# Kernel optimization log

Hardware: AMD Instinct MI355X
Metric: run time of the kernel (lower is better)

## Reference

```python
import jax, jax.numpy as jnp
import numpy as np


def setup_inputs() -> dict:
    key = jax.random.key(0)
    ks = jax.random.split(key, 7)
    B, D, N, R = 256, 5120, 16, 160  # batch, d_inner, d_state, dt_rank
    x = jax.random.normal(ks[0], (B, D), jnp.float32)
    h0 = jax.random.normal(ks[1], (B, D, N), jnp.float32)
    W_x_dt = jax.random.normal(ks[2], (D, R), jnp.float32) * (1.0 / np.sqrt(D))
    W_dt = jax.random.normal(ks[3], (R, D), jnp.float32) * (1.0 / np.sqrt(R))
    b_dt = jax.random.normal(ks[4], (D,), jnp.float32)
    W_BC = jax.random.normal(ks[5], (D, 2 * N), jnp.float32) * (1.0 / np.sqrt(D))
    A_log = jax.random.normal(ks[6], (D, N), jnp.float32)
    return {"x": x, "h0": h0, "W_x_dt": W_x_dt, "W_dt": W_dt,
            "b_dt": b_dt, "W_BC": W_BC, "A_log": A_log}


def reference(x, h0, W_x_dt, W_dt, b_dt, W_BC, A_log):
    # Single-token Mamba selective SSM step (batch dims squeezed: x [B,D], h0 [B,D,N]).
    N = A_log.shape[1]
    # delta_t = softplus(dt_proj(delta_t_proj(x)))  -> [B, D]
    dt = jax.nn.softplus((x @ W_x_dt) @ W_dt + b_dt)
    # BC projection, split into B and C parts -> [B, N] each
    BC = x @ W_BC
    Bm, Cm = BC[:, :N], BC[:, N:]
    A = -jnp.exp(A_log)                              # [D, N]
    delta_A = jnp.exp(A[None, :, :] * dt[:, :, None])   # [B, D, N]
    delta_Bx = (dt * x)[:, :, None] * Bm[:, None, :]     # [B, D, N]
    h = delta_A * h0 + delta_Bx                          # new hidden state
    # y = h @ C (per-batch bmm over state dim) + x residual
    y = jnp.einsum('bdn,bn->bd', h, Cm) + x              # [B, D]
    return y
```

## Files before the change

### kernel.cpp

```cpp
#include <hip/hip_runtime.h>
#include <math.h>

#define BB 256
#define DD 5120
#define NN 16
#define RR 160
#define CT 192
#define NSPLIT 32
#define TMP_ELEMS (BB * CT)
#define NEGA_ELEMS (DD * NN)

__global__ __launch_bounds__(256) void k1_gemm(const float* __restrict__ x,
                                               const float* __restrict__ Wxdt,
                                               const float* __restrict__ Wbc,
                                               float* __restrict__ part) {
    __shared__ float xs[32][68];
    __shared__ float ws[32][64];
    const int tid = threadIdx.x;
    const int tx = tid & 15, ty = tid >> 4;
    const int c0 = blockIdx.x * 64;
    const int b0 = blockIdx.y * 64;
    const int k0 = blockIdx.z * 160;
    float acc[4][4] = {};

    for (int kc = 0; kc < 160; kc += 32) {
        {
            const int i  = tid >> 3;
            const int j4 = (tid & 7) * 4;
            #pragma unroll
            for (int rep = 0; rep < 2; ++rep) {
                const int row = i + rep * 32;
                const float4 v = *(const float4*)&x[(size_t)(b0 + row) * DD + k0 + kc + j4];
                xs[j4 + 0][row] = v.x;
                xs[j4 + 1][row] = v.y;
                xs[j4 + 2][row] = v.z;
                xs[j4 + 3][row] = v.w;
            }
        }
        {
            const int c4 = (tid & 15) * 4;
            const int r0 = tid >> 4;
            #pragma unroll
            for (int rep = 0; rep < 2; ++rep) {
                const int r  = r0 + rep * 16;
                const int kg = k0 + kc + r;
                const int cg = c0 + c4;
                float4 v;
                if (cg < RR) v = *(const float4*)&Wxdt[(size_t)kg * RR + cg];
                else         v = *(const float4*)&Wbc[(size_t)kg * 32 + (cg - RR)];
                *(float4*)&ws[r][c4] = v;
            }
        }
        __syncthreads();
        #pragma unroll
        for (int k = 0; k < 32; ++k) {
            const float4 a4 = *(const float4*)&xs[k][ty * 4];
            const float4 w4 = *(const float4*)&ws[k][tx * 4];
            const float av[4] = {a4.x, a4.y, a4.z, a4.w};
            const float wv[4] = {w4.x, w4.y, w4.z, w4.w};
            #pragma unroll
            for (int u = 0; u < 4; ++u)
                #pragma unroll
                for (int v = 0; v < 4; ++v)
                    acc[u][v] = fmaf(av[u], wv[v], acc[u][v]);
        }
        __syncthreads();
    }

    float* p = part + (size_t)blockIdx.z * TMP_ELEMS;
    #pragma unroll
    for (int u = 0; u < 4; ++u) {
        const int b = b0 + ty * 4 + u;
        *(float4*)&p[b * CT + c0 + tx * 4] =
            make_float4(acc[u][0], acc[u][1], acc[u][2], acc[u][3]);
    }
}

__global__ __launch_bounds__(256) void k_red(const float* __restrict__ part,
                                             const float* __restrict__ Alog,
                                             float* __restrict__ tmp,
                                             float* __restrict__ negA) {
    const int idx = blockIdx.x * 256 + threadIdx.x;
    if (idx < TMP_ELEMS) {
        float s = 0.f;
        #pragma unroll
        for (int z = 0; z < NSPLIT; ++z) s += part[(size_t)z * TMP_ELEMS + idx];
        tmp[idx] = s;
    } else {
        const int j = idx - TMP_ELEMS;
        negA[j] = -__expf(Alog[j]);
    }
}

__global__ __launch_bounds__(256) void k_fused(const float* __restrict__ x,
                                               const float* __restrict__ h0,
                                               const float* __restrict__ Wdt,
                                               const float* __restrict__ bdt,
                                               const float* __restrict__ tmp,
                                               const float* __restrict__ negA,
                                               float* __restrict__ out) {
    const int tid = threadIdx.x;
    const int b0 = blockIdx.x * 4;
    const int d0 = blockIdx.y * 256;
    const int d  = d0 + tid;
    const float* wcol = Wdt + d;

    float acc[4] = {0.f, 0.f, 0.f, 0.f};
    #pragma unroll 4
    for (int k4 = 0; k4 < RR; k4 += 4) {
        const float w0 = wcol[(size_t)(k4 + 0) * DD];
        const float w1 = wcol[(size_t)(k4 + 1) * DD];
        const float w2 = wcol[(size_t)(k4 + 2) * DD];
        const float w3 = wcol[(size_t)(k4 + 3) * DD];
        #pragma unroll
        for (int bi = 0; bi < 4; ++bi) {
            const float4 t4 = *(const float4*)&tmp[(size_t)(b0 + bi) * CT + k4];
            acc[bi] = fmaf(t4.x, w0, acc[bi]);
            acc[bi] = fmaf(t4.y, w1, acc[bi]);
            acc[bi] = fmaf(t4.z, w2, acc[bi]);
            acc[bi] = fmaf(t4.w, w3, acc[bi]);
        }
    }

    const float bdv = bdt[d];
    float dtv[4];
    #pragma unroll
    for (int bi = 0; bi < 4; ++bi) {
        const float z = acc[bi] + bdv;
        dtv[bi] = fmaxf(z, 0.f) + log1pf(__expf(-fabsf(z)));
    }

    float av[16];
    {
        const float* ap = &negA[(size_t)d * NN];
        #pragma unroll
        for (int n4 = 0; n4 < NN; n4 += 4) {
            const float4 a4 = *(const float4*)&ap[n4];
            av[n4 + 0] = a4.x; av[n4 + 1] = a4.y;
            av[n4 + 2] = a4.z; av[n4 + 3] = a4.w;
        }
    }

    #pragma unroll
    for (int bi = 0; bi < 4; ++bi) {
        const size_t cell = (size_t)(b0 + bi) * DD + d;
        const float dt  = dtv[bi];
        const float xe  = x[cell];
        const float dtx = dt * xe;
        const float* hp  = &h0[cell * NN];
        const float* bmp = &tmp[(size_t)(b0 + bi) * CT + RR];
        float acc4[4] = {xe, 0.f, 0.f, 0.f};
        #pragma unroll
        for (int n4 = 0; n4 < NN; n4 += 4) {
            const float4 h4 = *(const float4*)&hp[n4];
            const float hv[4] = {h4.x, h4.y, h4.z, h4.w};
            #pragma unroll
            for (int q = 0; q < 4; ++q) {
                const int n = n4 + q;
                const float dA = __expf(av[n] * dt);
                const float h  = fmaf(dA, hv[q], dtx * bmp[n]);
                acc4[q] = fmaf(h, bmp[16 + n], acc4[q]);
            }
        }
        out[cell] = (acc4[0] + acc4[1]) + (acc4[2] + acc4[3]);
    }
}

extern "C" void kernel_launch(void* const* d_in, const int* in_sizes, int n_in,
                              void* d_out, int out_size, void* d_ws, size_t ws_size,
                              hipStream_t stream) {
    const float* x    = (const float*)d_in[0];
    const float* h0   = (const float*)d_in[1];
    const float* Wxdt = (const float*)d_in[2];
    const float* Wdt  = (const float*)d_in[3];
    const float* bdt  = (const float*)d_in[4];
    const float* Wbc  = (const float*)d_in[5];
    const float* Alog = (const float*)d_in[6];
    float* out = (float*)d_out;

    float* part = (float*)d_ws;
    float* tmp  = part + (size_t)NSPLIT * TMP_ELEMS;
    float* negA = tmp + TMP_ELEMS;

    k1_gemm<<<dim3(3, 4, NSPLIT), 256, 0, stream>>>(x, Wxdt, Wbc, part);
    k_red<<<dim3((TMP_ELEMS + NEGA_ELEMS) / 256), 256, 0, stream>>>(part, Alog, tmp, negA);
    k_fused<<<dim3(BB / 4, DD / 256), 256, 0, stream>>>(x, h0, Wdt, bdt, tmp, negA, out);
}
```

Baseline: 175.2 us.

## Replace LDS-tiled projection GEMM with register GEMV blocks and prefetch h0 early

The first projection kernel drops its shared-memory 64x64 tiling and instead gives each thread one output column over 8 batch rows, reading x as broadcast float4 loads and W columns directly. Its grid changes from 384 to 1024 blocks of 192 threads. The fused SSM kernel now issues the h0 and x loads before the dt_proj reduction loop, so the large h0 stream overlaps with the Wdt/tmp dot products. The cost is more register pressure from holding 64 h0 floats live, and some loss of data reuse in the first GEMM.

New measurement: 190.9 us. 1.09x slower.

```diff
diff --git a/kernel.cpp b/kernel.cpp
--- a/kernel.cpp
+++ b/kernel.cpp
@@ -7,73 +7,49 @@
 #define RR 160
 #define CT 192
 #define NSPLIT 32
+#define K1_KRANGE 160
 #define TMP_ELEMS (BB * CT)
 #define NEGA_ELEMS (DD * NN)
 
-__global__ __launch_bounds__(256) void k1_gemm(const float* __restrict__ x,
+__global__ __launch_bounds__(192) void k1_gemm(const float* __restrict__ x,
                                                const float* __restrict__ Wxdt,
                                                const float* __restrict__ Wbc,
                                                float* __restrict__ part) {
-    __shared__ float xs[32][68];
-    __shared__ float ws[32][64];
-    const int tid = threadIdx.x;
-    const int tx = tid & 15, ty = tid >> 4;
-    const int c0 = blockIdx.x * 64;
-    const int b0 = blockIdx.y * 64;
-    const int k0 = blockIdx.z * 160;
-    float acc[4][4] = {};
+    const int c  = threadIdx.x;
+    const int b0 = blockIdx.x * 8;
+    const int k0 = blockIdx.y * K1_KRANGE;
 
-    for (int kc = 0; kc < 160; kc += 32) {
-        {
-            const int i  = tid >> 3;
-            const int j4 = (tid & 7) * 4;
-            #pragma unroll
-            for (int rep = 0; rep < 2; ++rep) {
-                const int row = i + rep * 32;
-                const float4 v = *(const float4*)&x[(size_t)(b0 + row) * DD + k0 + kc + j4];
-                xs[j4 + 0][row] = v.x;
-                xs[j4 + 1][row] = v.y;
-                xs[j4 + 2][row] = v.z;
-                xs[j4 + 3][row] = v.w;
-            }
+    const bool isx = (c < RR);
+    const float* wp = isx ? (Wxdt + (size_t)k0 * RR + c)
+                          : (Wbc  + (size_t)k0 * 32 + (c - RR));
+    const int wstride = isx ? RR : 32;
+
+    float acc[8] = {};
+    for (int k8 = 0; k8 < K1_KRANGE; k8 += 8) {
+        float w[8];
+        #pragma unroll
+        for (int j = 0; j < 8; ++j) w[j] = wp[(size_t)j * wstride];
+        wp += (size_t)8 * wstride;
+        #pragma unroll
+        for (int bi = 0; bi < 8; ++bi) {
+            const float* xr = &x[(size_t)(b0 + bi) * DD + k0 + k8];
+            const float4 ta = *(const float4*)&xr[0];
+            const float4 tb = *(const float4*)&xr[4];
+            acc[bi] = fmaf(ta.x, w[0], acc[bi]);
+            acc[bi] = fmaf(ta.y, w[1], acc[bi]);
+            acc[bi] = fmaf(ta.z, w[2], acc[bi]);
+            acc[bi] = fmaf(ta.w, w[3], acc[bi]);
+            acc[bi] = fmaf(tb.x, w[4], acc[bi]);
+            acc[bi] = fmaf(tb.y, w[5], acc[bi]);
+            acc[bi] = fmaf(tb.z, w[6], acc[bi]);
+            acc[bi] = fmaf(tb.w, w[7], acc[bi]);
         }
-        {
-            const int c4 = (tid & 15) * 4;
-            const int r0 = tid >> 4;
-            #pragma unroll
-            for (int rep = 0; rep < 2; ++rep) {
-                const int r  = r0 + rep * 16;
-                const int kg = k0 + kc + r;
-                const int cg = c0 + c4;
-                float4 v;
-                if (cg < RR) v = *(const float4*)&Wxdt[(size_t)kg * RR + cg];
-                else         v = *(const float4*)&Wbc[(size_t)kg * 32 + (cg - RR)];
-                *(float4*)&ws[r][c4] = v;
-            }
-        }
-        __syncthreads();
-        #pragma unroll
-        for (int k = 0; k < 32; ++k) {
-            const float4 a4 = *(const float4*)&xs[k][ty * 4];
-            const float4 w4 = *(const float4*)&ws[k][tx * 4];
-            const float av[4] = {a4.x, a4.y, a4.z, a4.w};
-            const float wv[4] = {w4.x, w4.y, w4.z, w4.w};
-            #pragma unroll
-            for (int u = 0; u < 4; ++u)
-                #pragma unroll
-                for (int v = 0; v < 4; ++v)
-                    acc[u][v] = fmaf(av[u], wv[v], acc[u][v]);
-        }
-        __syncthreads();
     }
 
-    float* p = part + (size_t)blockIdx.z * TMP_ELEMS;
+    float* p = part + (size_t)blockIdx.y * TMP_ELEMS;
     #pragma unroll
-    for (int u = 0; u < 4; ++u) {
-        const int b = b0 + ty * 4 + u;
-        *(float4*)&p[b * CT + c0 + tx * 4] =
-            make_float4(acc[u][0], acc[u][1], acc[u][2], acc[u][3]);
-    }
+    for (int bi = 0; bi < 8; ++bi)
+        p[(b0 + bi) * CT + c] = acc[bi];
 }
 
 __global__ __launch_bounds__(256) void k_red(const float* __restrict__ part,
@@ -101,35 +77,18 @@
                                                float* __restrict__ out) {
     const int tid = threadIdx.x;
     const int b0 = blockIdx.x * 4;
-    const int d0 = blockIdx.y * 256;
-    const int d  = d0 + tid;
-    const float* wcol = Wdt + d;
+    const int d  = blockIdx.y * 256 + tid;
 
-    float acc[4] = {0.f, 0.f, 0.f, 0.f};
-    #pragma unroll 4
-    for (int k4 = 0; k4 < RR; k4 += 4) {
-        const float w0 = wcol[(size_t)(k4 + 0) * DD];
-        const float w1 = wcol[(size_t)(k4 + 1) * DD];
-        const float w2 = wcol[(size_t)(k4 + 2) * DD];
-        const float w3 = wcol[(size_t)(k4 + 3) * DD];
-        #pragma unroll
-        for (int bi = 0; bi < 4; ++bi) {
-            const float4 t4 = *(const float4*)&tmp[(size_t)(b0 + bi) * CT + k4];
-            acc[bi] = fmaf(t4.x, w0, acc[bi]);
-            acc[bi] = fmaf(t4.y, w1, acc[bi]);
-            acc[bi] = fmaf(t4.z, w2, acc[bi]);
-            acc[bi] = fmaf(t4.w, w3, acc[bi]);
-        }
-    }
-
-    const float bdv = bdt[d];
-    float dtv[4];
+    float4 h4[4][4];
+    float  xe[4];
     #pragma unroll
     for (int bi = 0; bi < 4; ++bi) {
-        const float z = acc[bi] + bdv;
-        dtv[bi] = fmaxf(z, 0.f) + log1pf(__expf(-fabsf(z)));
+        const size_t cell = (size_t)(b0 + bi) * DD + d;
+        xe[bi] = x[cell];
+        const float* hp = &h0[cell * NN];
+        #pragma unroll
+        for (int j = 0; j < 4; ++j) h4[bi][j] = *(const float4*)&hp[j * 4];
     }
-
     float av[16];
     {
         const float* ap = &negA[(size_t)d * NN];
@@ -140,29 +99,49 @@
             av[n4 + 2] = a4.z; av[n4 + 3] = a4.w;
         }
     }
+    const float bdv = bdt[d];
+
+    const float* wcol = Wdt + d;
+    float acc[4] = {0.f, 0.f, 0.f, 0.f};
+    for (int k8 = 0; k8 < RR; k8 += 8) {
+        float w[8];
+        #pragma unroll
+        for (int j = 0; j < 8; ++j) w[j] = wcol[(size_t)(k8 + j) * DD];
+        #pragma unroll
+        for (int bi = 0; bi < 4; ++bi) {
+            const float* tr = &tmp[(size_t)(b0 + bi) * CT + k8];
+            const float4 ta = *(const float4*)&tr[0];
+            const float4 tb = *(const float4*)&tr[4];
+            acc[bi] = fmaf(ta.x, w[0], acc[bi]);
+            acc[bi] = fmaf(ta.y, w[1], acc[bi]);
+            acc[bi] = fmaf(ta.z, w[2], acc[bi]);
+            acc[bi] = fmaf(ta.w, w[3], acc[bi]);
+            acc[bi] = fmaf(tb.x, w[4], acc[bi]);
+            acc[bi] = fmaf(tb.y, w[5], acc[bi]);
+            acc[bi] = fmaf(tb.z, w[6], acc[bi]);
+            acc[bi] = fmaf(tb.w, w[7], acc[bi]);
+        }
+    }
 
     #pragma unroll
     for (int bi = 0; bi < 4; ++bi) {
-        const size_t cell = (size_t)(b0 + bi) * DD + d;
-        const float dt  = dtv[bi];
-        const float xe  = x[cell];
-        const float dtx = dt * xe;
-        const float* hp  = &h0[cell * NN];
+        const float z  = acc[bi] + bdv;
+        const float dt = fmaxf(z, 0.f) + log1pf(__expf(-fabsf(z)));
+        const float dtx = dt * xe[bi];
         const float* bmp = &tmp[(size_t)(b0 + bi) * CT + RR];
-        float acc4[4] = {xe, 0.f, 0.f, 0.f};
+        float acc4[4] = {xe[bi], 0.f, 0.f, 0.f};
         #pragma unroll
-        for (int n4 = 0; n4 < NN; n4 += 4) {
-            const float4 h4 = *(const float4*)&hp[n4];
-            const float hv[4] = {h4.x, h4.y, h4.z, h4.w};
+        for (int j = 0; j < 4; ++j) {
+            const float hv[4] = {h4[bi][j].x, h4[bi][j].y, h4[bi][j].z, h4[bi][j].w};
             #pragma unroll
             for (int q = 0; q < 4; ++q) {
-                const int n = n4 + q;
+                const int n = j * 4 + q;
                 const float dA = __expf(av[n] * dt);
                 const float h  = fmaf(dA, hv[q], dtx * bmp[n]);
                 acc4[q] = fmaf(h, bmp[16 + n], acc4[q]);
             }
         }
-        out[cell] = (acc4[0] + acc4[1]) + (acc4[2] + acc4[3]);
+        out[(size_t)(b0 + bi) * DD + d] = (acc4[0] + acc4[1]) + (acc4[2] + acc4[3]);
     }
 }
 
@@ -182,7 +161,7 @@
     float* tmp  = part + (size_t)NSPLIT * TMP_ELEMS;
     float* negA = tmp + TMP_ELEMS;
 
-    k1_gemm<<<dim3(3, 4, NSPLIT), 256, 0, stream>>>(x, Wxdt, Wbc, part);
+    k1_gemm<<<dim3(BB / 8, NSPLIT), 192, 0, stream>>>(x, Wxdt, Wbc, part);
     k_red<<<dim3((TMP_ELEMS + NEGA_ELEMS) / 256), 256, 0, stream>>>(part, Alog, tmp, negA);
     k_fused<<<dim3(BB / 4, DD / 256), 256, 0, stream>>>(x, h0, Wdt, bdt, tmp, negA, out);
 }
```
